# Kernel tuning notes

Hardware: AMD Instinct MI355X
Metric: run time of the kernel (lower is better)

Reference implementation:

```python
import jax, jax.numpy as jnp
import numpy as np

B, T, D, H = 4096, 48, 64, 128
IMPUTE_WEIGHT = 0.3


def setup_inputs() -> dict:
    key = jax.random.key(0)
    ks = jax.random.split(key, 16)
    values = jax.random.normal(ks[0], (B, T, D), dtype=jnp.float32)
    masks = (jax.random.uniform(ks[1], (B, T, D)) < 0.7).astype(jnp.float32)
    deltas = jax.random.uniform(ks[2], (B, T, D), dtype=jnp.float32)
    s = 0.05
    return {
        "values": values, "masks": masks, "deltas": deltas,
        # TemporalDecay h (non-diag): Linear(D -> H)
        "W_td_h": jax.random.normal(ks[3], (H, D), dtype=jnp.float32) * s,
        "b_td_h": jax.random.normal(ks[4], (H,), dtype=jnp.float32) * s,
        # TemporalDecay x (diag): W is D x D but only diagonal used
        "W_td_x": jax.random.normal(ks[5], (D, D), dtype=jnp.float32) * s,
        "b_td_x": jax.random.normal(ks[6], (D,), dtype=jnp.float32) * s,
        # hist_reg: Linear(H -> D)
        "W_hist": jax.random.normal(ks[7], (D, H), dtype=jnp.float32) * s,
        "b_hist": jax.random.normal(ks[8], (D,), dtype=jnp.float32) * s,
        # feat_reg: D x D with zeroed diagonal mask
        "W_feat": jax.random.normal(ks[9], (D, D), dtype=jnp.float32) * s,
        "b_feat": jax.random.normal(ks[10], (D,), dtype=jnp.float32) * s,
        # weight_combine: Linear(2D -> D)
        "W_comb": jax.random.normal(ks[11], (D, 2 * D), dtype=jnp.float32) * s,
        "b_comb": jax.random.normal(ks[12], (D,), dtype=jnp.float32) * s,
        # LSTMCell(2D -> H), torch gate order i,f,g,o
        "W_ih": jax.random.normal(ks[13], (4 * H, 2 * D), dtype=jnp.float32) * s,
        "W_hh": jax.random.normal(ks[14], (4 * H, H), dtype=jnp.float32) * s,
        "b_ih": jnp.zeros((4 * H,), dtype=jnp.float32),
        "b_hh": jnp.zeros((4 * H,), dtype=jnp.float32),
    }


def reference(values, masks, deltas, W_td_h, b_td_h, W_td_x, b_td_x,
              W_hist, b_hist, W_feat, b_feat, W_comb, b_comb,
              W_ih, W_hh, b_ih, b_hh):
    Bn, Tn, Dn = values.shape
    Hn = W_hh.shape[1]
    w_td_x_diag = jnp.diagonal(W_td_x)                      # diag mask -> elementwise
    W_feat_m = W_feat * (1.0 - jnp.eye(Dn, dtype=W_feat.dtype))  # zero diagonal

    def step(carry, xs):
        h, c, x_loss = carry
        x, m, d = xs                                        # each [B, D]
        gamma_h = jnp.exp(-jax.nn.relu(d @ W_td_h.T + b_td_h))   # [B, H]
        gamma_x = jnp.exp(-jax.nn.relu(d * w_td_x_diag + b_td_x))  # [B, D]
        h = h * gamma_h
        x_h = h @ W_hist.T + b_hist
        denom = jnp.sum(m) + 1e-5
        x_loss = x_loss + jnp.sum(jnp.abs(x - x_h) * m) / denom
        x_c = m * x + (1.0 - m) * x_h
        z_h = x_c @ W_feat_m.T + b_feat
        x_loss = x_loss + jnp.sum(jnp.abs(x - z_h) * m) / denom
        alpha = jnp.concatenate([gamma_x, m], axis=1) @ W_comb.T + b_comb
        c_h = alpha * z_h + (1.0 - alpha) * x_h
        x_loss = x_loss + jnp.sum(jnp.abs(x - c_h) * m) / denom
        c_c = m * x + (1.0 - m) * c_h
        inp = jnp.concatenate([c_c, m], axis=1)             # [B, 2D]
        gates = inp @ W_ih.T + b_ih + h @ W_hh.T + b_hh     # [B, 4H]
        i_g, f_g, g_g, o_g = jnp.split(gates, 4, axis=1)
        c = jax.nn.sigmoid(f_g) * c + jax.nn.sigmoid(i_g) * jnp.tanh(g_g)
        h = jax.nn.sigmoid(o_g) * jnp.tanh(c)
        return (h, c, x_loss), c_c

    h0 = jnp.zeros((Bn, Hn), dtype=values.dtype)
    c0 = jnp.zeros((Bn, Hn), dtype=values.dtype)
    xs = (jnp.swapaxes(values, 0, 1), jnp.swapaxes(masks, 0, 1), jnp.swapaxes(deltas, 0, 1))
    (_, _, x_loss), imps = jax.lax.scan(step, (h0, c0, jnp.float32(0.0)), xs)
    imputations = jnp.swapaxes(imps, 0, 1)                  # [B, T, D]
    loss = x_loss * IMPUTE_WEIGHT
    return loss, imputations
```

## Files before the change

### kernel.cpp

```cpp
#include <hip/hip_runtime.h>
#include <cmath>

#define Bb 4096
#define Tt 48
#define Dd 64
#define Hh 128
#define NB 16
#define NTHR 512

typedef unsigned short ushort_t;
typedef __attribute__((ext_vector_type(8))) short short8;
typedef __attribute__((ext_vector_type(4))) float floatx4;
typedef __attribute__((ext_vector_type(4))) unsigned int uintx4;

#define WS_DEN   0
#define WS_LOSS  48
#define WS_FRAGS 64
#define FR_F 0
#define FR_A 256
#define FR_B 272
#define FR_C 288
#define FR_E 296
#define N_FRAGS 312

__device__ __forceinline__ ushort_t f2bf(float x) {
  unsigned int u = __float_as_uint(x);
  u += 0x7fffu + ((u >> 16) & 1u);
  return (ushort_t)(u >> 16);
}
__device__ __forceinline__ float sigmoidf_(float x) { return 1.0f / (1.0f + __expf(-x)); }
__device__ __forceinline__ float tanhf_(float x) { return 2.0f / (1.0f + __expf(-2.0f * x)) - 1.0f; }

__global__ void prep_kernel(const float* __restrict__ W_td_h, const float* __restrict__ W_hist,
                            const float* __restrict__ W_feat, const float* __restrict__ W_comb,
                            const float* __restrict__ W_ih, const float* __restrict__ W_hh,
                            float* __restrict__ ws) {
  int f = blockIdx.x;
  int tid = threadIdx.x;
  if (f == 0 && tid < 64) ws[tid] = 0.0f;
  ushort_t* fb = (ushort_t*)(ws + WS_FRAGS);
  #pragma unroll
  for (int u = 0; u < 2; u++) {
    int e = tid * 2 + u;
    int l = e >> 3, j = e & 7;
    int n16 = l & 15;
    int kq = ((l >> 4) << 3) + j;
    float v;
    if (f < 256) {
      int w = f >> 5, g = (f >> 3) & 3, ks = f & 7;
      int n = g * 128 + w * 16 + n16;
      int k = ks * 32 + kq;
      v = (k < 128) ? W_ih[n * 128 + k] : W_hh[n * 128 + (k - 128)];
    } else if (f < 272) {
      int ff = f - 256, w = ff >> 1, ks = ff & 1;
      int n = w * 16 + n16;
      v = W_td_h[n * 64 + ks * 32 + kq];
    } else if (f < 288) {
      int ff = f - 272, w = ff >> 2, ks = ff & 3;
      int n = w * 16 + n16;
      v = W_hist[n * 128 + ks * 32 + kq];
    } else if (f < 296) {
      int ff = f - 288, w = ff >> 1, ks = ff & 1;
      int n = w * 16 + n16;
      int k = ks * 32 + kq;
      v = (n == k) ? 0.0f : W_feat[n * 64 + k];
    } else {
      int ff = f - 296, w = ff >> 2, ks = ff & 3;
      int n = w * 16 + n16;
      v = W_comb[n * 128 + ks * 32 + kq];
    }
    fb[f * 512 + e] = f2bf(v);
  }
}

__global__ void denom_kernel(const float* __restrict__ masks, float* __restrict__ ws) {
  int t = blockIdx.x >> 4;
  int chunk = blockIdx.x & 15;
  int base = chunk * 256;
  int tid = threadIdx.x;
  int j = tid & 63;
  int brow = tid >> 6;
  float s = 0.0f;
  for (int i = 0; i < 64; i++) {
    int b = base + i * 4 + brow;
    s += masks[((size_t)b * Tt + t) * Dd + j];
  }
  for (int off = 32; off > 0; off >>= 1) s += __shfl_down(s, off, 64);
  __shared__ float red[4];
  if ((tid & 63) == 0) red[tid >> 6] = s;
  __syncthreads();
  if (tid == 0) atomicAdd(&ws[WS_DEN + t], red[0] + red[1] + red[2] + red[3]);
}

__global__ __launch_bounds__(NTHR, 2)
void main_kernel(const float* __restrict__ values, const float* __restrict__ masks,
                 const float* __restrict__ deltas, const float* __restrict__ W_td_x,
                 const float* __restrict__ b_td_h, const float* __restrict__ b_td_x,
                 const float* __restrict__ b_hist, const float* __restrict__ b_feat,
                 const float* __restrict__ b_comb,
                 const float* __restrict__ b_ih, const float* __restrict__ b_hh,
                 float* ws, float* __restrict__ out) {
  __shared__ __align__(16) ushort_t act[16 * 264];
  __shared__ __align__(16) ushort_t dbuf[16 * 72];
  __shared__ __align__(16) ushort_t gmbuf[16 * 136];
  __shared__ __align__(16) ushort_t xcbuf[16 * 72];
  __shared__ __align__(16) float xbuf[16 * 68];
  __shared__ __align__(16) float mbuf[16 * 68];
  __shared__ __align__(16) float xhbuf[16 * 68];
  __shared__ __align__(16) float zhbuf[16 * 68];
  __shared__ __align__(16) ushort_t fragA[16 * 512];
  __shared__ __align__(16) ushort_t fragC[8 * 512];
  __shared__ float red[8];

  int tid = threadIdx.x;
  int w = tid >> 6;
  int lane = tid & 63;
  int l15 = lane & 15;
  int quad = lane >> 4;
  int b0 = blockIdx.x * NB;
  const ushort_t* fb = (const ushort_t*)(ws + WS_FRAGS);

  {
    const uintx4* srcA = (const uintx4*)(fb + FR_A * 512);
    uintx4* dstA = (uintx4*)fragA;
    for (int i = tid; i < 1024; i += NTHR) dstA[i] = srcA[i];
    const uintx4* srcC = (const uintx4*)(fb + FR_C * 512);
    uintx4* dstC = (uintx4*)fragC;
    for (int i = tid; i < 512; i += NTHR) dstC[i] = srcC[i];
  }

  short8 wF[32];
  #pragma unroll
  for (int g = 0; g < 4; g++)
    #pragma unroll
    for (int ks = 0; ks < 8; ks++)
      wF[g * 8 + ks] = *(const short8*)(fb + (size_t)(FR_F + w * 32 + g * 8 + ks) * 512 + lane * 8);
  short8 wBE[4];
  if (w < 4) {
    #pragma unroll
    for (int ks = 0; ks < 4; ks++)
      wBE[ks] = *(const short8*)(fb + (size_t)(FR_B + w * 4 + ks) * 512 + lane * 8);
  } else {
    #pragma unroll
    for (int ks = 0; ks < 4; ks++)
      wBE[ks] = *(const short8*)(fb + (size_t)(FR_E + (w - 4) * 4 + ks) * 512 + lane * 8);
  }

  int colh = w * 16 + l15;
  float biasF0 = b_ih[colh]       + b_hh[colh];
  float biasF1 = b_ih[128 + colh] + b_hh[128 + colh];
  float biasF2 = b_ih[256 + colh] + b_hh[256 + colh];
  float biasF3 = b_ih[384 + colh] + b_hh[384 + colh];
  float biasA  = b_td_h[colh];
  int colD = (w & 3) * 16 + l15;
  float biasBE = (w < 4) ? b_hist[colD] : b_comb[colD];
  float biasC  = b_feat[colD];

  int e0 = tid * 2;
  int lb = e0 >> 6, li = e0 & 63;
  size_t gbase = ((size_t)(b0 + lb) * Tt) * Dd + li;
  float diag0 = W_td_x[li * 64 + li], diag1 = W_td_x[(li + 1) * 64 + (li + 1)];
  float btx0 = b_td_x[li], btx1 = b_td_x[li + 1];

  float h_reg[4] = {0.f, 0.f, 0.f, 0.f};
  float c_reg[4] = {0.f, 0.f, 0.f, 0.f};
  float loss_acc = 0.0f;
  float* imp = out + 1;

  for (int t = 0; t < Tt; t++) {
    __syncthreads();
    {
      size_t g = gbase + (size_t)t * Dd;
      float2 xv = *(const float2*)(values + g);
      float2 mv = *(const float2*)(masks + g);
      float2 dv = *(const float2*)(deltas + g);
      xbuf[lb * 68 + li] = xv.x; xbuf[lb * 68 + li + 1] = xv.y;
      mbuf[lb * 68 + li] = mv.x; mbuf[lb * 68 + li + 1] = mv.y;
      unsigned int mpk = (unsigned int)f2bf(mv.x) | ((unsigned int)f2bf(mv.y) << 16);
      *(unsigned int*)(&act[lb * 264 + 64 + li]) = mpk;
      *(unsigned int*)(&gmbuf[lb * 136 + 64 + li]) = mpk;
      *(unsigned int*)(&dbuf[lb * 72 + li]) =
          (unsigned int)f2bf(dv.x) | ((unsigned int)f2bf(dv.y) << 16);
      float g0 = __expf(-fmaxf(dv.x * diag0 + btx0, 0.0f));
      float g1 = __expf(-fmaxf(dv.y * diag1 + btx1, 0.0f));
      *(unsigned int*)(&gmbuf[lb * 136 + li]) =
          (unsigned int)f2bf(g0) | ((unsigned int)f2bf(g1) << 16);
    }
    float invden = 1.0f / (ws[WS_DEN + t] + 1e-5f);
    __syncthreads();

    {
      floatx4 acc = {biasA, biasA, biasA, biasA};
      #pragma unroll
      for (int ks = 0; ks < 2; ks++) {
        short8 a = *(const short8*)(&dbuf[l15 * 72 + ks * 32 + quad * 8]);
        short8 b = *(const short8*)(&fragA[(size_t)(w * 2 + ks) * 512 + lane * 8]);
        acc = __builtin_amdgcn_mfma_f32_16x16x32_bf16(a, b, acc, 0, 0, 0);
      }
      #pragma unroll
      for (int r = 0; r < 4; r++) {
        int m = quad * 4 + r;
        h_reg[r] *= __expf(-fmaxf(acc[r], 0.0f));
        act[m * 264 + 128 + colh] = f2bf(h_reg[r]);
      }
    }
    __syncthreads();

    floatx4 accP = {biasBE, biasBE, biasBE, biasBE};
    if (w < 4) {
      #pragma unroll
      for (int ks = 0; ks < 4; ks++) {
        short8 a = *(const short8*)(&act[l15 * 264 + 128 + ks * 32 + quad * 8]);
        accP = __builtin_amdgcn_mfma_f32_16x16x32_bf16(a, wBE[ks], accP, 0, 0, 0);
      }
      #pragma unroll
      for (int r = 0; r < 4; r++) {
        int m = quad * 4 + r;
        int ix = m * 68 + colD;
        float xh = accP[r];
        float xx = xbuf[ix], mm = mbuf[ix];
        loss_acc += fabsf(xx - xh) * mm * invden;
        xhbuf[ix] = xh;
        xcbuf[m * 72 + colD] = f2bf(mm * xx + (1.0f - mm) * xh);
      }
    } else {
      #pragma unroll
      for (int ks = 0; ks < 4; ks++) {
        short8 a = *(const short8*)(&gmbuf[l15 * 136 + ks * 32 + quad * 8]);
        accP = __builtin_amdgcn_mfma_f32_16x16x32_bf16(a, wBE[ks], accP, 0, 0, 0);
      }
    }
    __syncthreads();

    if (w < 4) {
      floatx4 acc = {biasC, biasC, biasC, biasC};
      #pragma unroll
      for (int ks = 0; ks < 2; ks++) {
        short8 a = *(const short8*)(&xcbuf[l15 * 72 + ks * 32 + quad * 8]);
        short8 b = *(const short8*)(&fragC[(size_t)(w * 2 + ks) * 512 + lane * 8]);
        acc = __builtin_amdgcn_mfma_f32_16x16x32_bf16(a, b, acc, 0, 0, 0);
      }
      #pragma unroll
      for (int r = 0; r < 4; r++) {
        int m = quad * 4 + r;
        int ix = m * 68 + colD;
        float zh = acc[r];
        loss_acc += fabsf(xbuf[ix] - zh) * mbuf[ix] * invden;
        zhbuf[ix] = zh;
      }
    }
    __syncthreads();

    if (w >= 4) {
      #pragma unroll
      for (int r = 0; r < 4; r++) {
        int m = quad * 4 + r;
        int ix = m * 68 + colD;
        float al = accP[r];
        float zh = zhbuf[ix], xh = xhbuf[ix];
        float xx = xbuf[ix], mm = mbuf[ix];
        float ch = al * zh + (1.0f - al) * xh;
        loss_acc += fabsf(xx - ch) * mm * invden;
        float cc = mm * xx + (1.0f - mm) * ch;
        imp[((size_t)(b0 + m) * Tt + t) * Dd + colD] = cc;
        act[m * 264 + colD] = f2bf(cc);
      }
    }
    __syncthreads();

    {
      floatx4 a0 = {biasF0, biasF0, biasF0, biasF0};
      floatx4 a1 = {biasF1, biasF1, biasF1, biasF1};
      floatx4 a2 = {biasF2, biasF2, biasF2, biasF2};
      floatx4 a3 = {biasF3, biasF3, biasF3, biasF3};
      #pragma unroll
      for (int ks = 0; ks < 8; ks++) {
        short8 a = *(const short8*)(&act[l15 * 264 + ks * 32 + quad * 8]);
        a0 = __builtin_amdgcn_mfma_f32_16x16x32_bf16(a, wF[ks], a0, 0, 0, 0);
        a1 = __builtin_amdgcn_mfma_f32_16x16x32_bf16(a, wF[8 + ks], a1, 0, 0, 0);
        a2 = __builtin_amdgcn_mfma_f32_16x16x32_bf16(a, wF[16 + ks], a2, 0, 0, 0);
        a3 = __builtin_amdgcn_mfma_f32_16x16x32_bf16(a, wF[24 + ks], a3, 0, 0, 0);
      }
      #pragma unroll
      for (int r = 0; r < 4; r++) {
        float ig = sigmoidf_(a0[r]);
        float fg = sigmoidf_(a1[r]);
        float gg = tanhf_(a2[r]);
        float og = sigmoidf_(a3[r]);
        c_reg[r] = fg * c_reg[r] + ig * gg;
        h_reg[r] = og * tanhf_(c_reg[r]);
      }
    }
  }

  float s = loss_acc;
  for (int off = 32; off > 0; off >>= 1) s += __shfl_down(s, off, 64);
  if (lane == 0) red[w] = s;
  __syncthreads();
  if (tid == 0) {
    float tot = 0.0f;
    #pragma unroll
    for (int i = 0; i < 8; i++) tot += red[i];
    atomicAdd(&ws[WS_LOSS], tot);
  }
}

__global__ void final_kernel(const float* __restrict__ ws, float* __restrict__ out) {
  if (threadIdx.x == 0 && blockIdx.x == 0) out[0] = 0.3f * ws[WS_LOSS];
}

extern "C" void kernel_launch(void* const* d_in, const int* in_sizes, int n_in,
                              void* d_out, int out_size, void* d_ws, size_t ws_size,
                              hipStream_t stream) {
  const float* values = (const float*)d_in[0];
  const float* masks  = (const float*)d_in[1];
  const float* deltas = (const float*)d_in[2];
  const float* W_td_h = (const float*)d_in[3];
  const float* b_td_h = (const float*)d_in[4];
  const float* W_td_x = (const float*)d_in[5];
  const float* b_td_x = (const float*)d_in[6];
  const float* W_hist = (const float*)d_in[7];
  const float* b_hist = (const float*)d_in[8];
  const float* W_feat = (const float*)d_in[9];
  const float* b_feat = (const float*)d_in[10];
  const float* W_comb = (const float*)d_in[11];
  const float* b_comb = (const float*)d_in[12];
  const float* W_ih   = (const float*)d_in[13];
  const float* W_hh   = (const float*)d_in[14];
  const float* b_ih   = (const float*)d_in[15];
  const float* b_hh   = (const float*)d_in[16];
  float* out = (float*)d_out;
  float* ws  = (float*)d_ws;

  prep_kernel<<<dim3(N_FRAGS), dim3(256), 0, stream>>>(W_td_h, W_hist, W_feat, W_comb,
                                                       W_ih, W_hh, ws);
  denom_kernel<<<dim3(48 * 16), dim3(256), 0, stream>>>(masks, ws);
  main_kernel<<<dim3(Bb / NB), dim3(NTHR), 0, stream>>>(values, masks, deltas, W_td_x,
                                                        b_td_h, b_td_x, b_hist, b_feat,
                                                        b_comb, b_ih, b_hh, ws, out);
  final_kernel<<<dim3(1), dim3(64), 0, stream>>>(ws, out);
}
```

Baseline: 376.6 us.

## Split LSTM gate GEMM across phases, prefetch inputs, keep weights in registers

The LSTM gate accumulation is split by K segment: the mask and hidden-state parts are issued early, interleaved with the decay and history MFMAs, and only the c_c part waits for the end. Next-step values, masks and deltas are prefetched into registers, and the td_h and feat weight fragments move from LDS into registers. The feat_reg and combine work moves to warps 4-7, which removes one barrier per timestep, and x and m are interleaved in a single LDS buffer. This cuts the serial latency of each recurrence step, but raises register pressure under launch_bounds(512,2), which could cause spills.

```diff
diff --git a/kernel.cpp b/kernel.cpp
--- a/kernel.cpp
+++ b/kernel.cpp
@@ -11,7 +11,6 @@
 typedef unsigned short ushort_t;
 typedef __attribute__((ext_vector_type(8))) short short8;
 typedef __attribute__((ext_vector_type(4))) float floatx4;
-typedef __attribute__((ext_vector_type(4))) unsigned int uintx4;
 
 #define WS_DEN   0
 #define WS_LOSS  48
@@ -102,14 +101,10 @@
                  float* ws, float* __restrict__ out) {
   __shared__ __align__(16) ushort_t act[16 * 264];
   __shared__ __align__(16) ushort_t dbuf[16 * 72];
-  __shared__ __align__(16) ushort_t gmbuf[16 * 136];
+  __shared__ __align__(16) ushort_t gxbuf[16 * 72];
   __shared__ __align__(16) ushort_t xcbuf[16 * 72];
-  __shared__ __align__(16) float xbuf[16 * 68];
-  __shared__ __align__(16) float mbuf[16 * 68];
+  __shared__ __align__(16) float xmbuf[16 * 132];
   __shared__ __align__(16) float xhbuf[16 * 68];
-  __shared__ __align__(16) float zhbuf[16 * 68];
-  __shared__ __align__(16) ushort_t fragA[16 * 512];
-  __shared__ __align__(16) ushort_t fragC[8 * 512];
   __shared__ float red[8];
 
   int tid = threadIdx.x;
@@ -120,22 +115,18 @@
   int b0 = blockIdx.x * NB;
   const ushort_t* fb = (const ushort_t*)(ws + WS_FRAGS);
 
-  {
-    const uintx4* srcA = (const uintx4*)(fb + FR_A * 512);
-    uintx4* dstA = (uintx4*)fragA;
-    for (int i = tid; i < 1024; i += NTHR) dstA[i] = srcA[i];
-    const uintx4* srcC = (const uintx4*)(fb + FR_C * 512);
-    uintx4* dstC = (uintx4*)fragC;
-    for (int i = tid; i < 512; i += NTHR) dstC[i] = srcC[i];
-  }
-
   short8 wF[32];
   #pragma unroll
   for (int g = 0; g < 4; g++)
     #pragma unroll
     for (int ks = 0; ks < 8; ks++)
       wF[g * 8 + ks] = *(const short8*)(fb + (size_t)(FR_F + w * 32 + g * 8 + ks) * 512 + lane * 8);
+  short8 wA[2];
+  #pragma unroll
+  for (int ks = 0; ks < 2; ks++)
+    wA[ks] = *(const short8*)(fb + (size_t)(FR_A + w * 2 + ks) * 512 + lane * 8);
   short8 wBE[4];
+  short8 wC[2];
   if (w < 4) {
     #pragma unroll
     for (int ks = 0; ks < 4; ks++)
@@ -144,6 +135,9 @@
     #pragma unroll
     for (int ks = 0; ks < 4; ks++)
       wBE[ks] = *(const short8*)(fb + (size_t)(FR_E + (w - 4) * 4 + ks) * 512 + lane * 8);
+    #pragma unroll
+    for (int ks = 0; ks < 2; ks++)
+      wC[ks] = *(const short8*)(fb + (size_t)(FR_C + (w - 4) * 2 + ks) * 512 + lane * 8);
   }
 
   int colh = w * 16 + l15;
@@ -162,125 +156,159 @@
   float diag0 = W_td_x[li * 64 + li], diag1 = W_td_x[(li + 1) * 64 + (li + 1)];
   float btx0 = b_td_x[li], btx1 = b_td_x[li + 1];
 
+  int ha[4];
+  float* impp[4];
+  #pragma unroll
+  for (int r = 0; r < 4; r++) {
+    int m = quad * 4 + r;
+    ha[r] = m * 264 + 128 + colh;
+    impp[r] = out + 1 + (size_t)(b0 + m) * Tt * Dd + colD;
+  }
+
   float h_reg[4] = {0.f, 0.f, 0.f, 0.f};
   float c_reg[4] = {0.f, 0.f, 0.f, 0.f};
   float loss_acc = 0.0f;
-  float* imp = out + 1;
+
+  float2 px = *(const float2*)(values + gbase);
+  float2 pm = *(const float2*)(masks + gbase);
+  float2 pd = *(const float2*)(deltas + gbase);
 
   for (int t = 0; t < Tt; t++) {
     __syncthreads();
+    *(float4*)(&xmbuf[lb * 132 + 2 * li]) = make_float4(px.x, pm.x, px.y, pm.y);
+    *(unsigned int*)(&act[lb * 264 + 64 + li]) =
+        (unsigned int)f2bf(pm.x) | ((unsigned int)f2bf(pm.y) << 16);
+    *(unsigned int*)(&dbuf[lb * 72 + li]) =
+        (unsigned int)f2bf(pd.x) | ((unsigned int)f2bf(pd.y) << 16);
+    float g0 = __expf(-fmaxf(pd.x * diag0 + btx0, 0.0f));
+    float g1 = __expf(-fmaxf(pd.y * diag1 + btx1, 0.0f));
+    *(unsigned int*)(&gxbuf[lb * 72 + li]) =
+        (unsigned int)f2bf(g0) | ((unsigned int)f2bf(g1) << 16);
+    float invden = 1.0f / (ws[WS_DEN + t] + 1e-5f);
+    floatx4 a0 = {biasF0, biasF0, biasF0, biasF0};
+    floatx4 a1 = {biasF1, biasF1, biasF1, biasF1};
+    floatx4 a2 = {biasF2, biasF2, biasF2, biasF2};
+    floatx4 a3 = {biasF3, biasF3, biasF3, biasF3};
     {
-      size_t g = gbase + (size_t)t * Dd;
-      float2 xv = *(const float2*)(values + g);
-      float2 mv = *(const float2*)(masks + g);
-      float2 dv = *(const float2*)(deltas + g);
-      xbuf[lb * 68 + li] = xv.x; xbuf[lb * 68 + li + 1] = xv.y;
-      mbuf[lb * 68 + li] = mv.x; mbuf[lb * 68 + li + 1] = mv.y;
-      unsigned int mpk = (unsigned int)f2bf(mv.x) | ((unsigned int)f2bf(mv.y) << 16);
-      *(unsigned int*)(&act[lb * 264 + 64 + li]) = mpk;
-      *(unsigned int*)(&gmbuf[lb * 136 + 64 + li]) = mpk;
-      *(unsigned int*)(&dbuf[lb * 72 + li]) =
-          (unsigned int)f2bf(dv.x) | ((unsigned int)f2bf(dv.y) << 16);
-      float g0 = __expf(-fmaxf(dv.x * diag0 + btx0, 0.0f));
-      float g1 = __expf(-fmaxf(dv.y * diag1 + btx1, 0.0f));
-      *(unsigned int*)(&gmbuf[lb * 136 + li]) =
-          (unsigned int)f2bf(g0) | ((unsigned int)f2bf(g1) << 16);
-    }
-    float invden = 1.0f / (ws[WS_DEN + t] + 1e-5f);
-    __syncthreads();
-
+      int tn = (t + 1 < Tt) ? (t + 1) : t;
+      size_t g = gbase + (size_t)tn * Dd;
+      px = *(const float2*)(values + g);
+      pm = *(const float2*)(masks + g);
+      pd = *(const float2*)(deltas + g);
+    }
+    __syncthreads();
+
+    short8 mf0 = *(const short8*)(&act[l15 * 264 + 64 + quad * 8]);
+    short8 mf1 = *(const short8*)(&act[l15 * 264 + 96 + quad * 8]);
     {
-      floatx4 acc = {biasA, biasA, biasA, biasA};
+      short8 df0 = *(const short8*)(&dbuf[l15 * 72 + quad * 8]);
+      short8 df1 = *(const short8*)(&dbuf[l15 * 72 + 32 + quad * 8]);
+      floatx4 accA = {biasA, biasA, biasA, biasA};
+      accA = __builtin_amdgcn_mfma_f32_16x16x32_bf16(df0, wA[0], accA, 0, 0, 0);
+      accA = __builtin_amdgcn_mfma_f32_16x16x32_bf16(df1, wA[1], accA, 0, 0, 0);
+      a0 = __builtin_amdgcn_mfma_f32_16x16x32_bf16(mf0, wF[2],  a0, 0, 0, 0);
+      a0 = __builtin_amdgcn_mfma_f32_16x16x32_bf16(mf1, wF[3],  a0, 0, 0, 0);
+      a1 = __builtin_amdgcn_mfma_f32_16x16x32_bf16(mf0, wF[10], a1, 0, 0, 0);
+      a1 = __builtin_amdgcn_mfma_f32_16x16x32_bf16(mf1, wF[11], a1, 0, 0, 0);
+      a2 = __builtin_amdgcn_mfma_f32_16x16x32_bf16(mf0, wF[18], a2, 0, 0, 0);
+      a2 = __builtin_amdgcn_mfma_f32_16x16x32_bf16(mf1, wF[19], a2, 0, 0, 0);
+      a3 = __builtin_amdgcn_mfma_f32_16x16x32_bf16(mf0, wF[26], a3, 0, 0, 0);
+      a3 = __builtin_amdgcn_mfma_f32_16x16x32_bf16(mf1, wF[27], a3, 0, 0, 0);
       #pragma unroll
-      for (int ks = 0; ks < 2; ks++) {
-        short8 a = *(const short8*)(&dbuf[l15 * 72 + ks * 32 + quad * 8]);
-        short8 b = *(const short8*)(&fragA[(size_t)(w * 2 + ks) * 512 + lane * 8]);
-        acc = __builtin_amdgcn_mfma_f32_16x16x32_bf16(a, b, acc, 0, 0, 0);
-      }
+      for (int r = 0; r < 4; r++) {
+        h_reg[r] *= __expf(-fmaxf(accA[r], 0.0f));
+        act[ha[r]] = f2bf(h_reg[r]);
+      }
+    }
+    __syncthreads();
+
+    floatx4 accP = {biasBE, biasBE, biasBE, biasBE};
+    {
+      short8 hf0 = *(const short8*)(&act[l15 * 264 + 128 + quad * 8]);
+      short8 hf1 = *(const short8*)(&act[l15 * 264 + 160 + quad * 8]);
+      short8 hf2 = *(const short8*)(&act[l15 * 264 + 192 + quad * 8]);
+      short8 hf3 = *(const short8*)(&act[l15 * 264 + 224 + quad * 8]);
+      if (w < 4) {
+        accP = __builtin_amdgcn_mfma_f32_16x16x32_bf16(hf0, wBE[0], accP, 0, 0, 0);
+        accP = __builtin_amdgcn_mfma_f32_16x16x32_bf16(hf1, wBE[1], accP, 0, 0, 0);
+        accP = __builtin_amdgcn_mfma_f32_16x16x32_bf16(hf2, wBE[2], accP, 0, 0, 0);
+        accP = __builtin_amdgcn_mfma_f32_16x16x32_bf16(hf3, wBE[3], accP, 0, 0, 0);
+      } else {
+        short8 gx0 = *(const short8*)(&gxbuf[l15 * 72 + quad * 8]);
+        short8 gx1 = *(const short8*)(&gxbuf[l15 * 72 + 32 + quad * 8]);
+        accP = __builtin_amdgcn_mfma_f32_16x16x32_bf16(gx0, wBE[0], accP, 0, 0, 0);
+        accP = __builtin_amdgcn_mfma_f32_16x16x32_bf16(gx1, wBE[1], accP, 0, 0, 0);
+        accP = __builtin_amdgcn_mfma_f32_16x16x32_bf16(mf0, wBE[2], accP, 0, 0, 0);
+        accP = __builtin_amdgcn_mfma_f32_16x16x32_bf16(mf1, wBE[3], accP, 0, 0, 0);
+      }
+      a0 = __builtin_amdgcn_mfma_f32_16x16x32_bf16(hf0, wF[4],  a0, 0, 0, 0);
+      a0 = __builtin_amdgcn_mfma_f32_16x16x32_bf16(hf1, wF[5],  a0, 0, 0, 0);
+      a0 = __builtin_amdgcn_mfma_f32_16x16x32_bf16(hf2, wF[6],  a0, 0, 0, 0);
+      a0 = __builtin_amdgcn_mfma_f32_16x16x32_bf16(hf3, wF[7],  a0, 0, 0, 0);
+      a1 = __builtin_amdgcn_mfma_f32_16x16x32_bf16(hf0, wF[12], a1, 0, 0, 0);
+      a1 = __builtin_amdgcn_mfma_f32_16x16x32_bf16(hf1, wF[13], a1, 0, 0, 0);
+      a1 = __builtin_amdgcn_mfma_f32_16x16x32_bf16(hf2, wF[14], a1, 0, 0, 0);
+      a1 = __builtin_amdgcn_mfma_f32_16x16x32_bf16(hf3, wF[15], a1, 0, 0, 0);
+      a2 = __builtin_amdgcn_mfma_f32_16x16x32_bf16(hf0, wF[20], a2, 0, 0, 0);
+      a2 = __builtin_amdgcn_mfma_f32_16x16x32_bf16(hf1, wF[21], a2, 0, 0, 0);
+      a2 = __builtin_amdgcn_mfma_f32_16x16x32_bf16(hf2, wF[22], a2, 0, 0, 0);
+      a2 = __builtin_amdgcn_mfma_f32_16x16x32_bf16(hf3, wF[23], a2, 0, 0, 0);
+      a3 = __builtin_amdgcn_mfma_f32_16x16x32_bf16(hf0, wF[28], a3, 0, 0, 0);
+      a3 = __builtin_amdgcn_mfma_f32_16x16x32_bf16(hf1, wF[29], a3, 0, 0, 0);
+      a3 = __builtin_amdgcn_mfma_f32_16x16x32_bf16(hf2, wF[30], a3, 0, 0, 0);
+      a3 = __builtin_amdgcn_mfma_f32_16x16x32_bf16(hf3, wF[31], a3, 0, 0, 0);
+      if (w < 4) {
+        #pragma unroll
+        for (int r = 0; r < 4; r++) {
+          int m = quad * 4 + r;
+          float2 xm = *(const float2*)(&xmbuf[m * 132 + 2 * colD]);
+          float xh = accP[r];
+          loss_acc += fabsf(xm.x - xh) * xm.y * invden;
+          xhbuf[m * 68 + colD] = xh;
+          xcbuf[m * 72 + colD] = f2bf(xm.y * xm.x + (1.0f - xm.y) * xh);
+        }
+      }
+    }
+    __syncthreads();
+
+    if (w >= 4) {
+      short8 xc0 = *(const short8*)(&xcbuf[l15 * 72 + quad * 8]);
+      short8 xc1 = *(const short8*)(&xcbuf[l15 * 72 + 32 + quad * 8]);
+      floatx4 accC = {biasC, biasC, biasC, biasC};
+      accC = __builtin_amdgcn_mfma_f32_16x16x32_bf16(xc0, wC[0], accC, 0, 0, 0);
+      accC = __builtin_amdgcn_mfma_f32_16x16x32_bf16(xc1, wC[1], accC, 0, 0, 0);
       #pragma unroll
       for (int r = 0; r < 4; r++) {
         int m = quad * 4 + r;
-        h_reg[r] *= __expf(-fmaxf(acc[r], 0.0f));
-        act[m * 264 + 128 + colh] = f2bf(h_reg[r]);
-      }
-    }
-    __syncthreads();
-
-    floatx4 accP = {biasBE, biasBE, biasBE, biasBE};
-    if (w < 4) {
-      #pragma unroll
-      for (int ks = 0; ks < 4; ks++) {
-        short8 a = *(const short8*)(&act[l15 * 264 + 128 + ks * 32 + quad * 8]);
-        accP = __builtin_amdgcn_mfma_f32_16x16x32_bf16(a, wBE[ks], accP, 0, 0, 0);
-      }
-      #pragma unroll
-      for (int r = 0; r < 4; r++) {
-        int m = quad * 4 + r;
-        int ix = m * 68 + colD;
-        float xh = accP[r];
-        float xx = xbuf[ix], mm = mbuf[ix];
-        loss_acc += fabsf(xx - xh) * mm * invden;
-        xhbuf[ix] = xh;
-        xcbuf[m * 72 + colD] = f2bf(mm * xx + (1.0f - mm) * xh);
+        float2 xm = *(const float2*)(&xmbuf[m * 132 + 2 * colD]);
+        float xh = xhbuf[m * 68 + colD];
+        float zh = accC[r];
+        float al = accP[r];
+        loss_acc += fabsf(xm.x - zh) * xm.y * invden;
+        float ch = al * zh + (1.0f - al) * xh;
+        loss_acc += fabsf(xm.x - ch) * xm.y * invden;
+        float cc = xm.y * xm.x + (1.0f - xm.y) * ch;
+        *impp[r] = cc;
+        impp[r] += Dd;
+        act[m * 264 + colD] = f2bf(cc);
       }
     } else {
       #pragma unroll
-      for (int ks = 0; ks < 4; ks++) {
-        short8 a = *(const short8*)(&gmbuf[l15 * 136 + ks * 32 + quad * 8]);
-        accP = __builtin_amdgcn_mfma_f32_16x16x32_bf16(a, wBE[ks], accP, 0, 0, 0);
-      }
-    }
-    __syncthreads();
-
-    if (w < 4) {
-      floatx4 acc = {biasC, biasC, biasC, biasC};
-      #pragma unroll
-      for (int ks = 0; ks < 2; ks++) {
-        short8 a = *(const short8*)(&xcbuf[l15 * 72 + ks * 32 + quad * 8]);
-        short8 b = *(const short8*)(&fragC[(size_t)(w * 2 + ks) * 512 + lane * 8]);
-        acc = __builtin_amdgcn_mfma_f32_16x16x32_bf16(a, b, acc, 0, 0, 0);
-      }
-      #pragma unroll
-      for (int r = 0; r < 4; r++) {
-        int m = quad * 4 + r;
-        int ix = m * 68 + colD;
-        float zh = acc[r];
-        loss_acc += fabsf(xbuf[ix] - zh) * mbuf[ix] * invden;
-        zhbuf[ix] = zh;
-      }
-    }
-    __syncthreads();
-
-    if (w >= 4) {
-      #pragma unroll
-      for (int r = 0; r < 4; r++) {
-        int m = quad * 4 + r;
-        int ix = m * 68 + colD;
-        float al = accP[r];
-        float zh = zhbuf[ix], xh = xhbuf[ix];
-        float xx = xbuf[ix], mm = mbuf[ix];
-        float ch = al * zh + (1.0f - al) * xh;
-        loss_acc += fabsf(xx - ch) * mm * invden;
-        float cc = mm * xx + (1.0f - mm) * ch;
-        imp[((size_t)(b0 + m) * Tt + t) * Dd + colD] = cc;
-        act[m * 264 + colD] = f2bf(cc);
-      }
+      for (int r = 0; r < 4; r++) impp[r] += Dd;
     }
     __syncthreads();
 
     {
-      floatx4 a0 = {biasF0, biasF0, biasF0, biasF0};
-      floatx4 a1 = {biasF1, biasF1, biasF1, biasF1};
-      floatx4 a2 = {biasF2, biasF2, biasF2, biasF2};
-      floatx4 a3 = {biasF3, biasF3, biasF3, biasF3};
-      #pragma unroll
-      for (int ks = 0; ks < 8; ks++) {
-        short8 a = *(const short8*)(&act[l15 * 264 + ks * 32 + quad * 8]);
-        a0 = __builtin_amdgcn_mfma_f32_16x16x32_bf16(a, wF[ks], a0, 0, 0, 0);
-        a1 = __builtin_amdgcn_mfma_f32_16x16x32_bf16(a, wF[8 + ks], a1, 0, 0, 0);
-        a2 = __builtin_amdgcn_mfma_f32_16x16x32_bf16(a, wF[16 + ks], a2, 0, 0, 0);
-        a3 = __builtin_amdgcn_mfma_f32_16x16x32_bf16(a, wF[24 + ks], a3, 0, 0, 0);
-      }
+      short8 cf0 = *(const short8*)(&act[l15 * 264 + quad * 8]);
+      short8 cf1 = *(const short8*)(&act[l15 * 264 + 32 + quad * 8]);
+      a0 = __builtin_amdgcn_mfma_f32_16x16x32_bf16(cf0, wF[0],  a0, 0, 0, 0);
+      a0 = __builtin_amdgcn_mfma_f32_16x16x32_bf16(cf1, wF[1],  a0, 0, 0, 0);
+      a1 = __builtin_amdgcn_mfma_f32_16x16x32_bf16(cf0, wF[8],  a1, 0, 0, 0);
+      a1 = __builtin_amdgcn_mfma_f32_16x16x32_bf16(cf1, wF[9],  a1, 0, 0, 0);
+      a2 = __builtin_amdgcn_mfma_f32_16x16x32_bf16(cf0, wF[16], a2, 0, 0, 0);
+      a2 = __builtin_amdgcn_mfma_f32_16x16x32_bf16(cf1, wF[17], a2, 0, 0, 0);
+      a3 = __builtin_amdgcn_mfma_f32_16x16x32_bf16(cf0, wF[24], a3, 0, 0, 0);
+      a3 = __builtin_amdgcn_mfma_f32_16x16x32_bf16(cf1, wF[25], a3, 0, 0, 0);
       #pragma unroll
       for (int r = 0; r < 4; r++) {
         float ig = sigmoidf_(a0[r]);
```

Result: no change. 375.2 us (-0.4%).
